# Optimization experiments

Measured on AMD Instinct MI355X. Metric: run time of the kernel, lower is better.

## Reference

```python
import jax, jax.numpy as jnp
import numpy as np

B, S, I, H = 64, 512, 512, 1024


def setup_inputs() -> dict:
    key = jax.random.key(0)
    ks = jax.random.split(key, 14)
    bound = (1.0 / H) ** 0.5

    def u(k, shape):
        return jax.random.uniform(k, shape, jnp.float32, -bound, bound)

    inp = {
        "inputs": jax.random.normal(ks[0], (B, S, I), jnp.float32),
        "hidden_states": jnp.zeros((1, B, H), jnp.float32),
        "w_ir": u(ks[1], (H, I)), "w_iz": u(ks[2], (H, I)), "w_in": u(ks[3], (H, I)),
        "b_ir": u(ks[4], (H,)), "b_iz": u(ks[5], (H,)), "b_in": u(ks[6], (H,)),
        "w_hr": u(ks[7], (H, H)), "w_hz": u(ks[8], (H, H)), "w_hn": u(ks[9], (H, H)),
        "b_hr": u(ks[10], (H,)), "b_hz": u(ks[11], (H,)), "b_hn": u(ks[12], (H,)),
    }
    return inp


def reference(inputs, hidden_states, w_ir, w_iz, w_in, b_ir, b_iz, b_in,
              w_hr, w_hz, w_hn, b_hr, b_hz, b_hn):
    h0 = hidden_states[0]  # [B, H]
    # Precompute all input-side projections once (batched GEMMs): [S, B, H]
    xr = (jnp.einsum("bsi,hi->sbh", inputs, w_ir) + b_ir)
    xz = (jnp.einsum("bsi,hi->sbh", inputs, w_iz) + b_iz)
    xn = (jnp.einsum("bsi,hi->sbh", inputs, w_in) + b_in)

    def step(h, xs):
        xr_t, xz_t, xn_t = xs
        r = jax.nn.sigmoid(xr_t + h @ w_hr.T + b_hr)
        z = jax.nn.sigmoid(xz_t + h @ w_hz.T + b_hz)
        n = jnp.tanh(xn_t + r * (h @ w_hn.T + b_hn))
        h_new = (1.0 - z) * n + z * h
        return h_new, h_new

    h_final, outs = jax.lax.scan(step, h0, (xr, xz, xn))  # outs: [S, B, H]
    outputs = jnp.transpose(outs, (1, 0, 2))  # [B, S, H]
    return outputs, h_final[None]
```

## Files before the change

kernel.cpp:

```cpp
#include <hip/hip_runtime.h>
#include <stdint.h>

typedef unsigned int u32;
typedef unsigned short u16;
typedef unsigned long long u64;
typedef __attribute__((ext_vector_type(8))) short short8;
typedef __attribute__((ext_vector_type(4))) float f32x4;

#define NB 64
#define NS 512
#define NI 512
#define NH 1024

#define OFF_AT    0ULL
#define OFF_WI    33554432ULL
#define OFF_WH    36700160ULL
#define OFF_XR    42991616ULL
#define OFF_XZ    110100480ULL
#define OFF_XN    177209344ULL
#define OFF_H     244318208ULL
#define OFF_FLAGS 244580352ULL

__device__ __forceinline__ u16 f2bf(float f){
  u32 u = __float_as_uint(f);
  u += 0x7fffu + ((u >> 16) & 1u);
  return (u16)(u >> 16);
}
__device__ __forceinline__ float bf2f(u16 h){
  return __uint_as_float(((u32)h) << 16);
}
__device__ __forceinline__ float sigm(float x){ return 1.0f / (1.0f + __expf(-x)); }
__device__ __forceinline__ float tanhf_(float x){
  float a = fabsf(x);
  float e = __expf(-2.0f * a);
  float t = (1.0f - e) / (1.0f + e);
  return copysignf(t, x);
}
__device__ __forceinline__ void gl_lds16(const void* g, void* l){
  __builtin_amdgcn_global_load_lds((const __attribute__((address_space(1))) void*)g,
                                   (__attribute__((address_space(3))) void*)l, 16, 0, 0);
}
__device__ __forceinline__ uint4 pack8(float4 a, float4 b){
  uint4 o;
  o.x = (u32)f2bf(a.x) | ((u32)f2bf(a.y) << 16);
  o.y = (u32)f2bf(a.z) | ((u32)f2bf(a.w) << 16);
  o.z = (u32)f2bf(b.x) | ((u32)f2bf(b.y) << 16);
  o.w = (u32)f2bf(b.z) | ((u32)f2bf(b.w) << 16);
  return o;
}
__device__ __forceinline__ u64 ald8(const u64* p){
  return __hip_atomic_load(p, __ATOMIC_RELAXED, __HIP_MEMORY_SCOPE_AGENT);
}
__device__ __forceinline__ void ast8(u64* p, u64 v){
  __hip_atomic_store(p, v, __ATOMIC_RELAXED, __HIP_MEMORY_SCOPE_AGENT);
}


__global__ void GRU_prep_at(const float* __restrict__ in, u16* __restrict__ at){
  int idx = blockIdx.x * 256 + threadIdx.x;
  int m = idx >> 6, k8 = idx & 63;
  int s = m >> 6, b = m & 63;
  const float* src = in + (((size_t)b * NS + s) * NI + k8 * 8);
  float4 f0 = *(const float4*)(src);
  float4 f1 = *(const float4*)(src + 4);
  uint4 o = pack8(f0, f1);
  *(uint4*)((char*)at + (size_t)m * 1024 + ((k8 * 16) ^ ((m & 7) << 4))) = o;
}

__global__ void GRU_prep_wi(const float* __restrict__ w0, const float* __restrict__ w1,
                            const float* __restrict__ w2, u16* __restrict__ wi){
  int idx = blockIdx.x * 256 + threadIdx.x;
  int g = idx >> 16;
  int rem = idx & 65535;
  int h = rem >> 6, k8 = rem & 63;
  const float* wsrc = (g == 0) ? w0 : ((g == 1) ? w1 : w2);
  const float* src = wsrc + (size_t)h * NI + k8 * 8;
  float4 f0 = *(const float4*)(src);
  float4 f1 = *(const float4*)(src + 4);
  uint4 o = pack8(f0, f1);
  *(uint4*)((char*)wi + ((size_t)(g * NH + h)) * 1024 + ((k8 * 16) ^ ((h & 7) << 4))) = o;
}

__global__ void GRU_prep_wh(const float* __restrict__ w0, const float* __restrict__ w1,
                            const float* __restrict__ w2, u16* __restrict__ wh){
  int idx = blockIdx.x * 256 + threadIdx.x;
  int l = idx & 63;
  int kc = (idx >> 6) & 31;
  int t = idx >> 11;
  int g = t >> 6, ft = t & 63;
  const float* wsrc = (g == 0) ? w0 : ((g == 1) ? w1 : w2);
  int f = ft * 16 + (l & 15);
  int k = kc * 32 + ((l >> 4) * 8);
  const float* src = wsrc + (size_t)f * NH + k;
  float4 f0 = *(const float4*)(src);
  float4 f1 = *(const float4*)(src + 4);
  uint4 o = pack8(f0, f1);
  *(uint4*)((char*)wh + (size_t)idx * 16) = o;
}

__global__ void GRU_init_h(const float* __restrict__ h0, u16* __restrict__ hImg,
                           u32* __restrict__ flags){
  int gt = blockIdx.x * 256 + threadIdx.x;
  if (gt < 8192){
    int b = gt >> 7, k8 = gt & 127;
    const float* src = h0 + (size_t)b * NH + k8 * 8;
    float4 f0 = *(const float4*)(src);
    float4 f1 = *(const float4*)(src + 4);
    uint4 o = pack8(f0, f1);
    *(uint4*)((char*)hImg + (size_t)b * 2048 + k8 * 16) = o;
  }
  if (gt < 64) flags[gt * 16] = 0;
}

__global__ __launch_bounds__(256) void GRU_xproj(const u16* __restrict__ AT,
    const u16* __restrict__ WI,
    const float* __restrict__ bi0, const float* __restrict__ bi1, const float* __restrict__ bi2,
    u16* __restrict__ xr, u16* __restrict__ xz, u16* __restrict__ xn){
  __shared__ __align__(16) char lds[32768];
  int tid = threadIdx.x;
  int l = tid & 63, w = tid >> 6;
  int c = l & 15, q = l >> 4;
  int mt = blockIdx.x, nt = blockIdx.y, g = blockIdx.z;
  const float* bi = (g == 0) ? bi0 : ((g == 1) ? bi1 : bi2);
  u16* xg = (g == 0) ? xr : ((g == 1) ? xz : xn);
  int m0 = mt * 128, n0 = nt * 128;
  int wm = w >> 1, wn = w & 1;

  f32x4 acc[4][4];
  #pragma unroll
  for (int i = 0; i < 4; ++i)
    #pragma unroll
    for (int j = 0; j < 4; ++j) acc[i][j] = (f32x4)0.0f;

  const char* Asrc = (const char*)AT + (size_t)m0 * 1024;
  const char* Bsrc = (const char*)WI + ((size_t)g * NH + n0) * 1024;

  for (int kt = 0; kt < 8; ++kt){
    #pragma unroll
    for (int r2 = 0; r2 < 4; ++r2){
      int idx = r2 * 256 + tid;
      int row = idx >> 3, k8 = idx & 7;
      gl_lds16(Asrc + (size_t)row * 1024 + kt * 128 + k8 * 16, lds + ((idx >> 6) << 10));
    }
    #pragma unroll
    for (int r2 = 0; r2 < 4; ++r2){
      int idx = r2 * 256 + tid;
      int row = idx >> 3, k8 = idx & 7;
      gl_lds16(Bsrc + (size_t)row * 1024 + kt * 128 + k8 * 16, lds + 16384 + ((idx >> 6) << 10));
    }
    __syncthreads();
    #pragma unroll
    for (int kk = 0; kk < 2; ++kk){
      short8 af[4], bf[4];
      int kb = kk * 64 + q * 16;
      #pragma unroll
      for (int mf = 0; mf < 4; ++mf){
        int row = wm * 64 + mf * 16 + c;
        af[mf] = *(const short8*)(lds + row * 128 + (kb ^ ((row & 7) << 4)));
      }
      #pragma unroll
      for (int nf = 0; nf < 4; ++nf){
        int row = wn * 64 + nf * 16 + c;
        bf[nf] = *(const short8*)(lds + 16384 + row * 128 + (kb ^ ((row & 7) << 4)));
      }
      #pragma unroll
      for (int mf = 0; mf < 4; ++mf)
        #pragma unroll
        for (int nf = 0; nf < 4; ++nf)
          acc[mf][nf] = __builtin_amdgcn_mfma_f32_16x16x32_bf16(af[mf], bf[nf], acc[mf][nf], 0, 0, 0);
    }
    __syncthreads();
  }
  int sidx = mt * 2 + wm;
  #pragma unroll
  for (int nf = 0; nf < 4; ++nf){
    int n = n0 + wn * 64 + nf * 16 + c;
    float bv = bi[n];
    #pragma unroll
    for (int mf = 0; mf < 4; ++mf){
      int b0 = mf * 16 + q * 4;
      u32 w0 = (u32)f2bf(acc[mf][nf][0] + bv) | ((u32)f2bf(acc[mf][nf][1] + bv) << 16);
      u32 w1 = (u32)f2bf(acc[mf][nf][2] + bv) | ((u32)f2bf(acc[mf][nf][3] + bv) << 16);
      uint2 o; o.x = w0; o.y = w1;
      *(uint2*)(xg + ((size_t)sidx * NH + n) * NB + b0) = o;
    }
  }
}

__global__ __launch_bounds__(256, 1) void GRU_rec(const u16* __restrict__ WH,
    const u16* __restrict__ xr, const u16* __restrict__ xz, const u16* __restrict__ xn,
    const float* __restrict__ bhr, const float* __restrict__ bhz, const float* __restrict__ bhn,
    const float* __restrict__ h0, u16* __restrict__ hImg, u32* __restrict__ flags,
    float* __restrict__ out){
  __shared__ __align__(16) char hl[34816];
  int tid = threadIdx.x;
  int l = tid & 63, w = tid >> 6;
  int wg = blockIdx.x;
  int bg = wg >> 4, fg = wg & 15;
  int c = l & 15, q = l >> 4;

  short8 bw[3][32];
  {
    const short8* base = (const short8*)WH;
    int ft = fg * 4 + w;
    #pragma unroll
    for (int g = 0; g < 3; ++g)
      #pragma unroll
      for (int kc = 0; kc < 32; ++kc)
        bw[g][kc] = base[(size_t)((g * 64 + ft) * 32 + kc) * 64 + l];
  }

  int frow = fg * 64 + w * 16 + c;
  int brow = bg * 16 + q * 4;
  float vbhr = bhr[frow], vbhz = bhz[frow], vbhn = bhn[frow];

  float hprev[4];
  #pragma unroll
  for (int j = 0; j < 4; ++j) hprev[j] = h0[(size_t)(brow + j) * NH + frow];

  char* hbytes = (char*)hImg;
  u32* myflag = flags + wg * 16;
  const u32* pollp = flags + (size_t)(bg * 16 + (l & 15)) * 16;
  int r = tid >> 4, ci = tid & 15;

  for (int s = 0; s < NS; ++s){
    u64 xrv, xzv, xnv;
    {
      size_t xo = ((size_t)s * NH + frow) * NB + brow;
      xrv = *(const u64*)(xr + xo);
      xzv = *(const u64*)(xz + xo);
      xnv = *(const u64*)(xn + xo);
    }
    if (s > 0){
      for (;;){
        u32 v = __hip_atomic_load(pollp, __ATOMIC_RELAXED, __HIP_MEMORY_SCOPE_AGENT);
        if (__all((int)(v >= (u32)s))) break;
      }
      __builtin_amdgcn_sched_barrier(0);
      asm volatile("" ::: "memory");
    }
    {
      const u64* hsrc = (const u64*)(hbytes + (size_t)(s & 1) * 131072)
                        + (size_t)(bg * 16 + r) * 256 + ci;
      u64 hv[16];
      #pragma unroll
      for (int e = 0; e < 16; ++e) hv[e] = ald8(hsrc + e * 16);
      char* dst = hl + r * 2048;
      #pragma unroll
      for (int e = 0; e < 16; ++e)
        *(u64*)(dst + ((e * 128 + ci * 8) ^ ((r & 7) << 4))) = hv[e];
    }
    __syncthreads();

    f32x4 ar0 = (f32x4)0.0f, ar1 = (f32x4)0.0f;
    f32x4 az0 = (f32x4)0.0f, az1 = (f32x4)0.0f;
    f32x4 an0 = (f32x4)0.0f, an1 = (f32x4)0.0f;
    #pragma unroll
    for (int kc = 0; kc < 32; kc += 2){
      short8 a0 = *(const short8*)(hl + c * 2048 + ((kc * 64 + q * 16) ^ ((c & 7) << 4)));
      short8 a1 = *(const short8*)(hl + c * 2048 + (((kc + 1) * 64 + q * 16) ^ ((c & 7) << 4)));
      ar0 = __builtin_amdgcn_mfma_f32_16x16x32_bf16(a0, bw[0][kc], ar0, 0, 0, 0);
      az0 = __builtin_amdgcn_mfma_f32_16x16x32_bf16(a0, bw[1][kc], az0, 0, 0, 0);
      an0 = __builtin_amdgcn_mfma_f32_16x16x32_bf16(a0, bw[2][kc], an0, 0, 0, 0);
      ar1 = __builtin_amdgcn_mfma_f32_16x16x32_bf16(a1, bw[0][kc + 1], ar1, 0, 0, 0);
      az1 = __builtin_amdgcn_mfma_f32_16x16x32_bf16(a1, bw[1][kc + 1], az1, 0, 0, 0);
      an1 = __builtin_amdgcn_mfma_f32_16x16x32_bf16(a1, bw[2][kc + 1], an1, 0, 0, 0);
    }
    f32x4 ar = ar0 + ar1, az = az0 + az1, an = an0 + an1;

    #pragma unroll
    for (int j = 0; j < 4; ++j){
      int b = brow + j;
      float rv = sigm(ar[j] + bf2f((u16)(xrv >> (16 * j))) + vbhr);
      float zv = sigm(az[j] + bf2f((u16)(xzv >> (16 * j))) + vbhz);
      float nv = tanhf_(bf2f((u16)(xnv >> (16 * j))) + rv * (an[j] + vbhn));
      float hn = (1.0f - zv) * nv + zv * hprev[j];
      hprev[j] = hn;
      out[((size_t)b * NS + s) * NH + frow] = hn;
      *(u16*)(hl + 32768 + (q * 4 + j) * 128 + (w * 16 + c) * 2) = f2bf(hn);
    }
    __syncthreads();
    {
      u64 tv = *(const u64*)(hl + 32768 + r * 128 + ci * 8);
      u64* hdst = (u64*)(hbytes + (size_t)((s + 1) & 1) * 131072)
                  + (size_t)(bg * 16 + r) * 256 + fg * 16 + ci;
      ast8(hdst, tv);
    }
    asm volatile("s_waitcnt vmcnt(0)" ::: "memory");
    __syncthreads();
    if (tid == 0)
      __hip_atomic_store(myflag, (u32)(s + 1), __ATOMIC_RELAXED, __HIP_MEMORY_SCOPE_AGENT);
  }
  #pragma unroll
  for (int j = 0; j < 4; ++j)
    out[(size_t)NB * NS * NH + (size_t)(brow + j) * NH + frow] = hprev[j];
}

extern "C" void kernel_launch(void* const* d_in, const int* in_sizes, int n_in,
                              void* d_out, int out_size, void* d_ws, size_t ws_size,
                              hipStream_t stream){
  const float* inputs = (const float*)d_in[0];
  const float* hidden = (const float*)d_in[1];
  const float* w_ir = (const float*)d_in[2];
  const float* w_iz = (const float*)d_in[3];
  const float* w_in = (const float*)d_in[4];
  const float* b_ir = (const float*)d_in[5];
  const float* b_iz = (const float*)d_in[6];
  const float* b_in = (const float*)d_in[7];
  const float* w_hr = (const float*)d_in[8];
  const float* w_hz = (const float*)d_in[9];
  const float* w_hn = (const float*)d_in[10];
  const float* b_hr = (const float*)d_in[11];
  const float* b_hz = (const float*)d_in[12];
  const float* b_hn = (const float*)d_in[13];

  char* ws = (char*)d_ws;
  u16* AT = (u16*)(ws + OFF_AT);
  u16* WI = (u16*)(ws + OFF_WI);
  u16* WH = (u16*)(ws + OFF_WH);
  u16* XR = (u16*)(ws + OFF_XR);
  u16* XZ = (u16*)(ws + OFF_XZ);
  u16* XN = (u16*)(ws + OFF_XN);
  u16* HIMG = (u16*)(ws + OFF_H);
  u32* FLAGS = (u32*)(ws + OFF_FLAGS);
  float* out = (float*)d_out;

  GRU_prep_at<<<dim3(8192), dim3(256), 0, stream>>>(inputs, AT);
  GRU_prep_wi<<<dim3(768), dim3(256), 0, stream>>>(w_ir, w_iz, w_in, WI);
  GRU_prep_wh<<<dim3(1536), dim3(256), 0, stream>>>(w_hr, w_hz, w_hn, WH);
  GRU_init_h<<<dim3(32), dim3(256), 0, stream>>>(hidden, HIMG, FLAGS);
  GRU_xproj<<<dim3(256, 8, 3), dim3(256), 0, stream>>>(AT, WI, b_ir, b_iz, b_in, XR, XZ, XN);
  GRU_rec<<<dim3(64), dim3(256), 0, stream>>>(WH, XR, XZ, XN, b_hr, b_hz, b_hn,
                                              hidden, HIMG, FLAGS, out);
}
```

Baseline: 2.448 ms.

## Replace flag-based inter-block sync with sentinel-polled hidden-state buffers

Measured after the change: 2.914 ms. +19.0%, slower.

```diff
diff --git a/kernel.cpp b/kernel.cpp
--- a/kernel.cpp
+++ b/kernel.cpp
@@ -12,14 +12,15 @@
 #define NI 512
 #define NH 1024
 
+#define SENT 0x7F807F807F807F80ULL
+
 #define OFF_AT    0ULL
+#define OFF_H     0ULL
 #define OFF_WI    33554432ULL
 #define OFF_WH    36700160ULL
 #define OFF_XR    42991616ULL
 #define OFF_XZ    110100480ULL
 #define OFF_XN    177209344ULL
-#define OFF_H     244318208ULL
-#define OFF_FLAGS 244580352ULL
 
 __device__ __forceinline__ u16 f2bf(float f){
   u32 u = __float_as_uint(f);
@@ -98,18 +99,20 @@
   *(uint4*)((char*)wh + (size_t)idx * 16) = o;
 }
 
-__global__ void GRU_init_h(const float* __restrict__ h0, u16* __restrict__ hImg,
-                           u32* __restrict__ flags){
+__global__ void GRU_init_h(const float* __restrict__ h0, u16* __restrict__ hImg){
   int gt = blockIdx.x * 256 + threadIdx.x;
-  if (gt < 8192){
-    int b = gt >> 7, k8 = gt & 127;
-    const float* src = h0 + (size_t)b * NH + k8 * 8;
-    float4 f0 = *(const float4*)(src);
-    float4 f1 = *(const float4*)(src + 4);
-    uint4 o = pack8(f0, f1);
-    *(uint4*)((char*)hImg + (size_t)b * 2048 + k8 * 16) = o;
-  }
-  if (gt < 64) flags[gt * 16] = 0;
+  int b = gt >> 7, k8 = gt & 127;
+  const float* src = h0 + (size_t)b * NH + k8 * 8;
+  float4 f0 = *(const float4*)(src);
+  float4 f1 = *(const float4*)(src + 4);
+  uint4 o = pack8(f0, f1);
+  *(uint4*)((char*)hImg + (size_t)b * 2048 + k8 * 16) = o;
+  u64* hb = (u64*)hImg;
+  #pragma unroll
+  for (int qb = 1; qb <= 3; ++qb){
+    hb[(size_t)qb * 16384 + (size_t)gt * 2 + 0] = SENT;
+    hb[(size_t)qb * 16384 + (size_t)gt * 2 + 1] = SENT;
+  }
 }
 
 __global__ __launch_bounds__(256) void GRU_xproj(const u16* __restrict__ AT,
@@ -190,9 +193,8 @@
 __global__ __launch_bounds__(256, 1) void GRU_rec(const u16* __restrict__ WH,
     const u16* __restrict__ xr, const u16* __restrict__ xz, const u16* __restrict__ xn,
     const float* __restrict__ bhr, const float* __restrict__ bhz, const float* __restrict__ bhn,
-    const float* __restrict__ h0, u16* __restrict__ hImg, u32* __restrict__ flags,
-    float* __restrict__ out){
-  __shared__ __align__(16) char hl[34816];
+    const float* __restrict__ h0, u16* __restrict__ hImg, float* __restrict__ out){
+  __shared__ __align__(16) char hl[68096];
   int tid = threadIdx.x;
   int l = tid & 63, w = tid >> 6;
   int wg = blockIdx.x;
@@ -219,11 +221,18 @@
   for (int j = 0; j < 4; ++j) hprev[j] = h0[(size_t)(brow + j) * NH + frow];
 
   char* hbytes = (char*)hImg;
-  u32* myflag = flags + wg * 16;
-  const u32* pollp = flags + (size_t)(bg * 16 + (l & 15)) * 16;
   int r = tid >> 4, ci = tid & 15;
+  int rb = l & 15, fo = l >> 4;
+  int gidx = fg * 16 + w * 4 + fo;
+  char* myT = hl + 65536 + w * 640;
 
   for (int s = 0; s < NS; ++s){
+    const u64* hsrc = (const u64*)(hbytes + (size_t)(s & 3) * 131072)
+                      + (size_t)(bg * 16 + r) * 256 + ci;
+    u64 hv[16];
+    #pragma unroll
+    for (int e = 0; e < 16; ++e) hv[e] = ald8(hsrc + e * 16);
+
     u64 xrv, xzv, xnv;
     {
       size_t xo = ((size_t)s * NH + frow) * NB + brow;
@@ -231,34 +240,38 @@
       xzv = *(const u64*)(xz + xo);
       xnv = *(const u64*)(xn + xo);
     }
-    if (s > 0){
-      for (;;){
-        u32 v = __hip_atomic_load(pollp, __ATOMIC_RELAXED, __HIP_MEMORY_SCOPE_AGENT);
-        if (__all((int)(v >= (u32)s))) break;
-      }
-      __builtin_amdgcn_sched_barrier(0);
-      asm volatile("" ::: "memory");
-    }
+
+    for (;;){
+      bool ok = true;
+      #pragma unroll
+      for (int e = 0; e < 16; ++e) ok &= (hv[e] != SENT);
+      if (ok) break;
+      #pragma unroll
+      for (int e = 0; e < 16; ++e)
+        if (hv[e] == SENT) hv[e] = ald8(hsrc + e * 16);
+    }
+
     {
-      const u64* hsrc = (const u64*)(hbytes + (size_t)(s & 1) * 131072)
-                        + (size_t)(bg * 16 + r) * 256 + ci;
-      u64 hv[16];
-      #pragma unroll
-      for (int e = 0; e < 16; ++e) hv[e] = ald8(hsrc + e * 16);
-      char* dst = hl + r * 2048;
+      char* dst = hl + (s & 1) * 32768 + r * 2048;
       #pragma unroll
       for (int e = 0; e < 16; ++e)
         *(u64*)(dst + ((e * 128 + ci * 8) ^ ((r & 7) << 4))) = hv[e];
     }
+    if (s >= 1){
+      u64* cdst = (u64*)(hbytes + (size_t)((s - 1) & 3) * 131072)
+                  + (size_t)(bg * 16 + rb) * 256 + gidx;
+      ast8(cdst, SENT);
+    }
     __syncthreads();
 
+    const char* hb0 = hl + (s & 1) * 32768;
     f32x4 ar0 = (f32x4)0.0f, ar1 = (f32x4)0.0f;
     f32x4 az0 = (f32x4)0.0f, az1 = (f32x4)0.0f;
     f32x4 an0 = (f32x4)0.0f, an1 = (f32x4)0.0f;
     #pragma unroll
     for (int kc = 0; kc < 32; kc += 2){
-      short8 a0 = *(const short8*)(hl + c * 2048 + ((kc * 64 + q * 16) ^ ((c & 7) << 4)));
-      short8 a1 = *(const short8*)(hl + c * 2048 + (((kc + 1) * 64 + q * 16) ^ ((c & 7) << 4)));
+      short8 a0 = *(const short8*)(hb0 + c * 2048 + ((kc * 64 + q * 16) ^ ((c & 7) << 4)));
+      short8 a1 = *(const short8*)(hb0 + c * 2048 + (((kc + 1) * 64 + q * 16) ^ ((c & 7) << 4)));
       ar0 = __builtin_amdgcn_mfma_f32_16x16x32_bf16(a0, bw[0][kc], ar0, 0, 0, 0);
       az0 = __builtin_amdgcn_mfma_f32_16x16x32_bf16(a0, bw[1][kc], az0, 0, 0, 0);
       an0 = __builtin_amdgcn_mfma_f32_16x16x32_bf16(a0, bw[2][kc], an0, 0, 0, 0);
@@ -268,28 +281,26 @@
     }
     f32x4 ar = ar0 + ar1, az = az0 + az1, an = an0 + an1;
 
+    float hn4[4];
     #pragma unroll
     for (int j = 0; j < 4; ++j){
-      int b = brow + j;
       float rv = sigm(ar[j] + bf2f((u16)(xrv >> (16 * j))) + vbhr);
       float zv = sigm(az[j] + bf2f((u16)(xzv >> (16 * j))) + vbhz);
       float nv = tanhf_(bf2f((u16)(xnv >> (16 * j))) + rv * (an[j] + vbhn));
       float hn = (1.0f - zv) * nv + zv * hprev[j];
       hprev[j] = hn;
-      out[((size_t)b * NS + s) * NH + frow] = hn;
-      *(u16*)(hl + 32768 + (q * 4 + j) * 128 + (w * 16 + c) * 2) = f2bf(hn);
-    }
-    __syncthreads();
+      hn4[j] = hn;
+      *(u16*)(myT + (q * 4 + j) * 40 + c * 2) = f2bf(hn);
+    }
     {
-      u64 tv = *(const u64*)(hl + 32768 + r * 128 + ci * 8);
-      u64* hdst = (u64*)(hbytes + (size_t)((s + 1) & 1) * 131072)
-                  + (size_t)(bg * 16 + r) * 256 + fg * 16 + ci;
+      u64 tv = *(const u64*)(myT + rb * 40 + fo * 8);
+      u64* hdst = (u64*)(hbytes + (size_t)((s + 1) & 3) * 131072)
+                  + (size_t)(bg * 16 + rb) * 256 + gidx;
       ast8(hdst, tv);
     }
-    asm volatile("s_waitcnt vmcnt(0)" ::: "memory");
-    __syncthreads();
-    if (tid == 0)
-      __hip_atomic_store(myflag, (u32)(s + 1), __ATOMIC_RELAXED, __HIP_MEMORY_SCOPE_AGENT);
+    #pragma unroll
+    for (int j = 0; j < 4; ++j)
+      out[((size_t)(brow + j) * NS + s) * NH + frow] = hn4[j];
   }
   #pragma unroll
   for (int j = 0; j < 4; ++j)
@@ -322,14 +333,13 @@
   u16* XZ = (u16*)(ws + OFF_XZ);
   u16* XN = (u16*)(ws + OFF_XN);
   u16* HIMG = (u16*)(ws + OFF_H);
-  u32* FLAGS = (u32*)(ws + OFF_FLAGS);
   float* out = (float*)d_out;
 
   GRU_prep_at<<<dim3(8192), dim3(256), 0, stream>>>(inputs, AT);
   GRU_prep_wi<<<dim3(768), dim3(256), 0, stream>>>(w_ir, w_iz, w_in, WI);
   GRU_prep_wh<<<dim3(1536), dim3(256), 0, stream>>>(w_hr, w_hz, w_hn, WH);
-  GRU_init_h<<<dim3(32), dim3(256), 0, stream>>>(hidden, HIMG, FLAGS);
   GRU_xproj<<<dim3(256, 8, 3), dim3(256), 0, stream>>>(AT, WI, b_ir, b_iz, b_in, XR, XZ, XN);
+  GRU_init_h<<<dim3(32), dim3(256), 0, stream>>>(hidden, HIMG);
   GRU_rec<<<dim3(64), dim3(256), 0, stream>>>(WH, XR, XZ, XN, b_hr, b_hz, b_hn,
-                                              hidden, HIMG, FLAGS, out);
-}
+                                              hidden, HIMG, out);
+}
```

## Pin recurrent batch groups to single XCDs with cache-scoped loads and flags

Applied to the files above, without the earlier changes.

After: 3.637 ms. +48.6%, slower.

```diff
diff --git a/kernel.cpp b/kernel.cpp
--- a/kernel.cpp
+++ b/kernel.cpp
@@ -13,13 +13,13 @@
 #define NH 1024
 
 #define OFF_AT    0ULL
+#define OFF_H     0ULL
 #define OFF_WI    33554432ULL
 #define OFF_WH    36700160ULL
 #define OFF_XR    42991616ULL
 #define OFF_XZ    110100480ULL
 #define OFF_XN    177209344ULL
-#define OFF_H     244318208ULL
-#define OFF_FLAGS 244580352ULL
+#define OFF_FLAGS 244318208ULL
 
 __device__ __forceinline__ u16 f2bf(float f){
   u32 u = __float_as_uint(f);
@@ -48,11 +48,25 @@
   o.w = (u32)f2bf(b.z) | ((u32)f2bf(b.w) << 16);
   return o;
 }
-__device__ __forceinline__ u64 ald8(const u64* p){
-  return __hip_atomic_load(p, __ATOMIC_RELAXED, __HIP_MEMORY_SCOPE_AGENT);
-}
-__device__ __forceinline__ void ast8(u64* p, u64 v){
-  __hip_atomic_store(p, v, __ATOMIC_RELAXED, __HIP_MEMORY_SCOPE_AGENT);
+
+__device__ __forceinline__ u32 ld4_mall(const u32* p){
+  u32 r;
+  asm volatile("global_load_dword %0, %1, off sc0 sc1\n\ts_waitcnt vmcnt(0)"
+               : "=v"(r) : "v"(p) : "memory");
+  return r;
+}
+__device__ __forceinline__ void st4_mall(u32* p, u32 v){
+  asm volatile("global_store_dword %0, %1, off sc0 sc1" :: "v"(p), "v"(v) : "memory");
+}
+__device__ __forceinline__ u64 ld8_l2(const void* p){
+  u64 r;
+  asm volatile("global_load_dwordx2 %0, %1, off sc0 nt" : "=v"(r) : "v"(p));
+  return r;
+}
+__device__ __forceinline__ u64 ld8_mall(const void* p){
+  u64 r;
+  asm volatile("global_load_dwordx2 %0, %1, off sc0 sc1" : "=v"(r) : "v"(p));
+  return r;
 }
 
 
@@ -109,7 +123,8 @@
     uint4 o = pack8(f0, f1);
     *(uint4*)((char*)hImg + (size_t)b * 2048 + k8 * 16) = o;
   }
-  if (gt < 64) flags[gt * 16] = 0;
+  if (gt < 256) flags[gt * 16] = 0;
+  if (gt >= 256 && gt < 264) flags[4096 + (gt - 256) * 16] = 0;
 }
 
 __global__ __launch_bounds__(256) void GRU_xproj(const u16* __restrict__ AT,
@@ -192,11 +207,22 @@
     const float* __restrict__ bhr, const float* __restrict__ bhz, const float* __restrict__ bhn,
     const float* __restrict__ h0, u16* __restrict__ hImg, u32* __restrict__ flags,
     float* __restrict__ out){
-  __shared__ __align__(16) char hl[34816];
+  __shared__ __align__(16) char hl[83968];
+
+  u32 xcd = (u32)__builtin_amdgcn_s_getreg(6164);
+  if (xcd >= 4) return;
+
   int tid = threadIdx.x;
+  int* roleS = (int*)(hl + 34816);
+  if (tid == 0)
+    *roleS = (int)__hip_atomic_fetch_add(flags + 4096 + xcd * 16, 1u,
+                                         __ATOMIC_RELAXED, __HIP_MEMORY_SCOPE_AGENT);
+  __syncthreads();
+  int role = *roleS;
+  if (role >= 16) return;
+
+  int bg = (int)xcd, fg = role;
   int l = tid & 63, w = tid >> 6;
-  int wg = blockIdx.x;
-  int bg = wg >> 4, fg = wg & 15;
   int c = l & 15, q = l >> 4;
 
   short8 bw[3][32];
@@ -219,9 +245,9 @@
   for (int j = 0; j < 4; ++j) hprev[j] = h0[(size_t)(brow + j) * NH + frow];
 
   char* hbytes = (char*)hImg;
-  u32* myflag = flags + wg * 16;
-  const u32* pollp = flags + (size_t)(bg * 16 + (l & 15)) * 16;
   int r = tid >> 4, ci = tid & 15;
+  u32* myflag = flags + (size_t)(bg * 16 + fg) * 16;
+  u32* pollp  = flags + (size_t)(bg * 16 + (l & 15)) * 16;
 
   for (int s = 0; s < NS; ++s){
     u64 xrv, xzv, xnv;
@@ -232,19 +258,26 @@
       xnv = *(const u64*)(xn + xo);
     }
     if (s > 0){
-      for (;;){
-        u32 v = __hip_atomic_load(pollp, __ATOMIC_RELAXED, __HIP_MEMORY_SCOPE_AGENT);
+      for (int it = 0; it < 4096; ++it){
+        u32 v = ld4_mall(pollp);
         if (__all((int)(v >= (u32)s))) break;
       }
       __builtin_amdgcn_sched_barrier(0);
-      asm volatile("" ::: "memory");
-    }
+    }
+
     {
-      const u64* hsrc = (const u64*)(hbytes + (size_t)(s & 1) * 131072)
-                        + (size_t)(bg * 16 + r) * 256 + ci;
+      const char* hsrc = hbytes + (size_t)(s & 1) * 131072
+                         + (size_t)(bg * 16 + r) * 2048 + ci * 8;
       u64 hv[16];
-      #pragma unroll
-      for (int e = 0; e < 16; ++e) hv[e] = ald8(hsrc + e * 16);
+      if (s == 0){
+        #pragma unroll
+        for (int e = 0; e < 16; ++e) hv[e] = ld8_mall(hsrc + e * 128);
+      } else {
+        #pragma unroll
+        for (int e = 0; e < 16; ++e) hv[e] = ld8_l2(hsrc + e * 128);
+      }
+      asm volatile("s_waitcnt vmcnt(0)" ::: "memory");
+      __builtin_amdgcn_sched_barrier(0);
       char* dst = hl + r * 2048;
       #pragma unroll
       for (int e = 0; e < 16; ++e)
@@ -268,29 +301,31 @@
     }
     f32x4 ar = ar0 + ar1, az = az0 + az1, an = an0 + an1;
 
+    float hn4[4];
     #pragma unroll
     for (int j = 0; j < 4; ++j){
-      int b = brow + j;
       float rv = sigm(ar[j] + bf2f((u16)(xrv >> (16 * j))) + vbhr);
       float zv = sigm(az[j] + bf2f((u16)(xzv >> (16 * j))) + vbhz);
       float nv = tanhf_(bf2f((u16)(xnv >> (16 * j))) + rv * (an[j] + vbhn));
       float hn = (1.0f - zv) * nv + zv * hprev[j];
       hprev[j] = hn;
-      out[((size_t)b * NS + s) * NH + frow] = hn;
+      hn4[j] = hn;
       *(u16*)(hl + 32768 + (q * 4 + j) * 128 + (w * 16 + c) * 2) = f2bf(hn);
     }
     __syncthreads();
     {
       u64 tv = *(const u64*)(hl + 32768 + r * 128 + ci * 8);
-      u64* hdst = (u64*)(hbytes + (size_t)((s + 1) & 1) * 131072)
-                  + (size_t)(bg * 16 + r) * 256 + fg * 16 + ci;
-      ast8(hdst, tv);
+      *(u64*)(hbytes + (size_t)((s + 1) & 1) * 131072
+              + (size_t)(bg * 16 + r) * 2048 + (size_t)(fg * 16 + ci) * 8) = tv;
     }
     asm volatile("s_waitcnt vmcnt(0)" ::: "memory");
     __syncthreads();
-    if (tid == 0)
-      __hip_atomic_store(myflag, (u32)(s + 1), __ATOMIC_RELAXED, __HIP_MEMORY_SCOPE_AGENT);
-  }
+    if (tid == 0) st4_mall(myflag, (u32)(s + 1));
+    #pragma unroll
+    for (int j = 0; j < 4; ++j)
+      out[((size_t)(brow + j) * NS + s) * NH + frow] = hn4[j];
+  }
+
   #pragma unroll
   for (int j = 0; j < 4; ++j)
     out[(size_t)NB * NS * NH + (size_t)(brow + j) * NH + frow] = hprev[j];
@@ -328,8 +363,8 @@
   GRU_prep_at<<<dim3(8192), dim3(256), 0, stream>>>(inputs, AT);
   GRU_prep_wi<<<dim3(768), dim3(256), 0, stream>>>(w_ir, w_iz, w_in, WI);
   GRU_prep_wh<<<dim3(1536), dim3(256), 0, stream>>>(w_hr, w_hz, w_hn, WH);
+  GRU_xproj<<<dim3(256, 8, 3), dim3(256), 0, stream>>>(AT, WI, b_ir, b_iz, b_in, XR, XZ, XN);
   GRU_init_h<<<dim3(32), dim3(256), 0, stream>>>(hidden, HIMG, FLAGS);
-  GRU_xproj<<<dim3(256, 8, 3), dim3(256), 0, stream>>>(AT, WI, b_ir, b_iz, b_in, XR, XZ, XN);
-  GRU_rec<<<dim3(64), dim3(256), 0, stream>>>(WH, XR, XZ, XN, b_hr, b_hz, b_hn,
-                                              hidden, HIMG, FLAGS, out);
-}
+  GRU_rec<<<dim3(1024), dim3(256), 0, stream>>>(WH, XR, XZ, XN, b_hr, b_hz, b_hn,
+                                                hidden, HIMG, FLAGS, out);
+}
```
